# Optimization experiments

Measured on AMD Instinct MI355X. Metric: run time of the kernel, lower is better.

## Reference

```python
import jax, jax.numpy as jnp
import numpy as np

B, T, I, H, O = 128, 512, 128, 256, 1

def setup_inputs() -> dict:
    key = jax.random.key(0)
    ks = jax.random.split(key, 7)
    s_ih = 1.0 / np.sqrt(H)
    return {
        "x": jax.random.normal(ks[0], (B, T, I), dtype=jnp.float32),
        "W_ih": jax.random.uniform(ks[1], (H, I), minval=-s_ih, maxval=s_ih, dtype=jnp.float32),
        "W_hh": jax.random.uniform(ks[2], (H, H), minval=-s_ih, maxval=s_ih, dtype=jnp.float32),
        "b_ih": jax.random.uniform(ks[3], (H,), minval=-s_ih, maxval=s_ih, dtype=jnp.float32),
        "b_hh": jax.random.uniform(ks[4], (H,), minval=-s_ih, maxval=s_ih, dtype=jnp.float32),
        "W_fc": jax.random.uniform(ks[5], (O, H), minval=-s_ih, maxval=s_ih, dtype=jnp.float32),
        "b_fc": jax.random.uniform(ks[6], (O,), minval=-s_ih, maxval=s_ih, dtype=jnp.float32),
    }

def reference(x, W_ih, W_hh, b_ih, b_hh, W_fc, b_fc):
    # Precompute input projections for all timesteps: [B, T, H]
    xp = jnp.einsum("bti,hi->bth", x, W_ih) + b_ih + b_hh
    h0 = jnp.zeros((x.shape[0], W_hh.shape[0]), dtype=x.dtype)

    def step(h, xp_t):
        h_new = jnp.tanh(xp_t + h @ W_hh.T)
        return h_new, None

    # scan over time axis; only final hidden state is needed
    h_last, _ = jax.lax.scan(step, h0, jnp.swapaxes(xp, 0, 1))
    logits = h_last @ W_fc.T + b_fc
    return jax.nn.sigmoid(logits)
```

## Files before the change

kernel.cpp:

```cpp
#include <hip/hip_runtime.h>
#include <hip/hip_bf16.h>


#define B_ 128
#define T_ 512
#define I_ 128
#define H_ 256
#define SCALE 2.8853900817779268f
#define WSC 2032.0f
#define HSC 127.0f
#define SCOMB (SCALE / (WSC * HSC))

typedef __attribute__((ext_vector_type(8))) short short8;
typedef __attribute__((ext_vector_type(4))) float floatx4;
typedef __attribute__((ext_vector_type(4))) int int4v;

__device__ __forceinline__ short8 pack8(float4 lo, float4 hi) {
    __hip_bfloat162 p0 = __float22bfloat162_rn(float2{lo.x, lo.y});
    __hip_bfloat162 p1 = __float22bfloat162_rn(float2{lo.z, lo.w});
    __hip_bfloat162 p2 = __float22bfloat162_rn(float2{hi.x, hi.y});
    __hip_bfloat162 p3 = __float22bfloat162_rn(float2{hi.z, hi.w});
    int4 i;
    i.x = *(int*)&p0; i.y = *(int*)&p1; i.z = *(int*)&p2; i.w = *(int*)&p3;
    return *(short8*)&i;
}
__device__ __forceinline__ short8 pack8s(float4 lo, float4 hi, float s) {
    lo.x *= s; lo.y *= s; lo.z *= s; lo.w *= s;
    hi.x *= s; hi.y *= s; hi.z *= s; hi.w *= s;
    return pack8(lo, hi);
}
__device__ __forceinline__ float tanh_s(float v) {
    float e = __builtin_amdgcn_exp2f(v);
    float r = __builtin_amdgcn_rcpf(e + 1.0f);
    return __builtin_fmaf(-2.0f, r, 1.0f);
}
__device__ __forceinline__ int q4(float a, float b, float c, float d, float s) {
    int qa = (int)rintf(a * s) & 255;
    int qb = (int)rintf(b * s) & 255;
    int qc = (int)rintf(c * s) & 255;
    int qd = (int)rintf(d * s) & 255;
    return qa | (qb << 8) | (qc << 16) | (qd << 24);
}

#define XP_GRID 256
#define XP_NT   ((B_ * T_ / 16) / XP_GRID)
__global__ __launch_bounds__(256, 1)
void xp_kernel(const float* __restrict__ x, const float* __restrict__ W_ih,
               const float* __restrict__ b_ih, const float* __restrict__ b_hh,
               float* __restrict__ xp) {
    const int tid  = threadIdx.x;
    const int wave = tid >> 6, lane = tid & 63;
    const int l15  = lane & 15, quad = lane >> 4;
    const int n0   = wave * 64;

    short8 wfrag[4][4];
#pragma unroll
    for (int mtt = 0; mtt < 4; ++mtt)
#pragma unroll
        for (int kq = 0; kq < 4; ++kq) {
            const float* p = W_ih + (long)(n0 + mtt * 16 + l15) * I_ + kq * 32 + quad * 8;
            wfrag[mtt][kq] = pack8s(*(const float4*)p, *(const float4*)(p + 4), SCALE);
        }
    floatx4 biasv[4];
#pragma unroll
    for (int mtt = 0; mtt < 4; ++mtt)
#pragma unroll
        for (int r = 0; r < 4; ++r) {
            int n = n0 + mtt * 16 + quad * 4 + r;
            biasv[mtt][r] = SCALE * (b_ih[n] + b_hh[n]);
        }

    const long mbase = (long)blockIdx.x * XP_NT * 16;

    float4 qa[4][2], qb[4][2];
#define LDX(Q, IT)                                                              \
    {                                                                           \
        const int itc = ((IT) < XP_NT) ? (IT) : (XP_NT - 1);                    \
        const float* p = x + (mbase + (long)itc * 16 + l15) * I_ + quad * 8;    \
        _Pragma("unroll")                                                       \
        for (int kq = 0; kq < 4; ++kq) {                                        \
            Q[kq][0] = *(const float4*)(p + kq * 32);                           \
            Q[kq][1] = *(const float4*)(p + kq * 32 + 4);                       \
        }                                                                       \
    }
#define ITER(Q, IT, ILD)                                                        \
    {                                                                           \
        short8 xf[4];                                                           \
        _Pragma("unroll")                                                       \
        for (int kq = 0; kq < 4; ++kq) xf[kq] = pack8(Q[kq][0], Q[kq][1]);      \
        LDX(Q, ILD);                                                            \
        floatx4 acc[4];                                                         \
        _Pragma("unroll")                                                       \
        for (int mtt = 0; mtt < 4; ++mtt) acc[mtt] = biasv[mtt];                \
        _Pragma("unroll")                                                       \
        for (int kq = 0; kq < 4; ++kq)                                          \
            _Pragma("unroll")                                                   \
            for (int mtt = 0; mtt < 4; ++mtt)                                   \
                acc[mtt] = __builtin_amdgcn_mfma_f32_16x16x32_bf16(             \
                    wfrag[mtt][kq], xf[kq], acc[mtt], 0, 0, 0);                 \
        float* o = xp + (mbase + (long)(IT) * 16 + l15) * H_ + n0 + quad * 4;   \
        _Pragma("unroll")                                                       \
        for (int mtt = 0; mtt < 4; ++mtt) {                                     \
            float4 st = {acc[mtt][0], acc[mtt][1], acc[mtt][2], acc[mtt][3]};   \
            *(float4*)(o + mtt * 16) = st;                                      \
        }                                                                       \
    }

    LDX(qa, 0);
    LDX(qb, 1);
#pragma unroll 1
    for (int it = 0; it < XP_NT; it += 2) {
        ITER(qa, it, it + 2);
        ITER(qb, it + 1, it + 3);
    }
#undef ITER
#undef LDX
}

__global__ __launch_bounds__(512, 2)
void rnn_kernel(const float* __restrict__ xp, const float* __restrict__ W_hh,
                const float* __restrict__ W_fc, const float* __restrict__ b_fc,
                float* __restrict__ out) {
    __shared__ __align__(16) signed char hbuf[2][16][256];
    const int tid  = threadIdx.x;
    const int wave = tid >> 6, lane = tid & 63;
    const int l15  = lane & 15, quad = lane >> 4;
    const int b0   = blockIdx.x * 16;
    const int n0   = wave * 32;
    const int swz  = l15 & 7;

    int4v wfrag[2][4];
#pragma unroll
    for (int mt = 0; mt < 2; ++mt)
#pragma unroll
        for (int kq = 0; kq < 4; ++kq) {
            const float* p = W_hh + (long)(n0 + mt * 16 + l15) * H_ + kq * 64 + quad * 16;
            int4v f;
#pragma unroll
            for (int j = 0; j < 4; ++j) {
                float4 w = *(const float4*)(p + j * 4);
                f[j] = q4(w.x, w.y, w.z, w.w, WSC);
            }
            wfrag[mt][kq] = f;
        }

    {
        int* hz = (int*)&hbuf[0][0][0];
#pragma unroll
        for (int i = tid; i < 2 * 16 * 256 / 4; i += 512) hz[i] = 0;
    }

    int roff[4];
#pragma unroll
    for (int kq = 0; kq < 4; ++kq)
        roff[kq] = l15 * 256 + (((kq * 4 + quad) ^ swz) << 4);
    int woff[2];
#pragma unroll
    for (int mt = 0; mt < 2; ++mt) {
        int c = wave * 2 + mt;
        woff[mt] = l15 * 256 + ((c ^ swz) << 4) + quad * 4;
    }

    const float* xpl = xp + (long)(b0 + l15) * T_ * H_ + n0 + quad * 4;
    float4 xvA0 = *(const float4*)(xpl);
    float4 xvA1 = *(const float4*)(xpl + 16);
    float4 xvB0 = *(const float4*)(xpl + H_);
    float4 xvB1 = *(const float4*)(xpl + H_ + 16);

    __syncthreads();

    const signed char* hb0r = &hbuf[0][0][0]; signed char* hb0w = &hbuf[0][0][0];
    const signed char* hb1r = &hbuf[1][0][0]; signed char* hb1w = &hbuf[1][0][0];

#define BAR() asm volatile("s_waitcnt lgkmcnt(0)\n\ts_barrier" ::: "memory")

#define STEP(HR, HW, XV0, XV1, TLD)                                             \
    {                                                                           \
                  \
        int4v hfrag[4];                                                         \
        _Pragma("unroll")                                                       \
        for (int kq = 0; kq < 4; ++kq)                                          \
            hfrag[kq] = *(const int4v*)((HR) + roff[kq]);                       \
               \
        float4 xc0 = XV0, xc1 = XV1;                                            \
        XV0 = *(const float4*)(xpl + (long)(TLD) * H_);                         \
        XV1 = *(const float4*)(xpl + (long)(TLD) * H_ + 16);                    \
                                    \
        int4v aC[2], aZ[2];                                                     \
        _Pragma("unroll")                                                       \
        for (int mt = 0; mt < 2; ++mt) {                                        \
            aC[mt] = (int4v){0, 0, 0, 0};                                       \
            aZ[mt] = (int4v){0, 0, 0, 0};                                       \
        }                                                                       \
        _Pragma("unroll")                                                       \
        for (int mt = 0; mt < 2; ++mt) {                                        \
            aC[mt] = __builtin_amdgcn_mfma_i32_16x16x64_i8(                     \
                wfrag[mt][0], hfrag[0], aC[mt], 0, 0, 0);                       \
            aZ[mt] = __builtin_amdgcn_mfma_i32_16x16x64_i8(                     \
                wfrag[mt][2], hfrag[2], aZ[mt], 0, 0, 0);                       \
            aC[mt] = __builtin_amdgcn_mfma_i32_16x16x64_i8(                     \
                wfrag[mt][1], hfrag[1], aC[mt], 0, 0, 0);                       \
            aZ[mt] = __builtin_amdgcn_mfma_i32_16x16x64_i8(                     \
                wfrag[mt][3], hfrag[3], aZ[mt], 0, 0, 0);                       \
        }                                                                       \
             \
        _Pragma("unroll")                                                       \
        for (int mt = 0; mt < 2; ++mt) {                                        \
            float4 xc = (mt == 0) ? xc0 : xc1;                                  \
            float r0 = tanh_s(__builtin_fmaf((float)(aC[mt][0] + aZ[mt][0]), SCOMB, xc.x)); \
            float r1 = tanh_s(__builtin_fmaf((float)(aC[mt][1] + aZ[mt][1]), SCOMB, xc.y)); \
            float r2 = tanh_s(__builtin_fmaf((float)(aC[mt][2] + aZ[mt][2]), SCOMB, xc.z)); \
            float r3 = tanh_s(__builtin_fmaf((float)(aC[mt][3] + aZ[mt][3]), SCOMB, xc.w)); \
            *(int*)((HW) + woff[mt]) = q4(r0, r1, r2, r3, HSC);                 \
        }                                                                       \
        BAR();                                                                  \
    }

#pragma unroll 1
    for (int t = 0; t < T_; t += 2) {
        const int tl0 = (t + 2 < T_) ? t + 2 : T_ - 1;
        const int tl1 = (t + 3 < T_) ? t + 3 : T_ - 1;
        STEP(hb0r, hb1w, xvA0, xvA1, tl0);
        STEP(hb1r, hb0w, xvB0, xvB1, tl1);
    }
#undef STEP
#undef BAR

    if (tid < 256) {
        const int bl = tid >> 4, seg = tid & 15;
        const int bswz = bl & 7;
        const signed char* hr = &hbuf[0][0][0] + bl * 256 + ((seg ^ bswz) << 4);
        float p = 0.0f;
#pragma unroll
        for (int i = 0; i < 16; ++i)
            p += (float)hr[i] * W_fc[seg * 16 + i];
#pragma unroll
        for (int off = 1; off < 16; off <<= 1) p += __shfl_xor(p, off);
        if (seg == 0)
            out[b0 + bl] = 1.0f / (1.0f + __expf(-(p * (1.0f / HSC) + b_fc[0])));
    }
}

extern "C" void kernel_launch(void* const* d_in, const int* in_sizes, int n_in,
                              void* d_out, int out_size, void* d_ws, size_t ws_size,
                              hipStream_t stream) {
    const float* x    = (const float*)d_in[0];
    const float* W_ih = (const float*)d_in[1];
    const float* W_hh = (const float*)d_in[2];
    const float* b_ih = (const float*)d_in[3];
    const float* b_hh = (const float*)d_in[4];
    const float* W_fc = (const float*)d_in[5];
    const float* b_fc = (const float*)d_in[6];
    float* out = (float*)d_out;

    float* xp = (float*)d_ws;

    xp_kernel<<<XP_GRID, 256, 0, stream>>>(x, W_ih, b_ih, b_hh, xp);
    rnn_kernel<<<B_ / 16, 512, 0, stream>>>(xp, W_hh, W_fc, b_fc, out);
}
```

Before: 396.0 us.

## Pre-quantize input projection to int32 MFMA accumulator scale and fuse tanh-quantize

The input projection is now stored as int32 values pre-scaled by the weight times hidden quantization scale, so the recurrent step can seed the int8 MFMA accumulator directly with it. This removes the separate aZ accumulator chain, the per-element float add, and the fmaf in the serial loop. The tanh plus int8 quantization is fused into one fma using a magic-number float trick, with byte extraction done via v_perm instead of rintf, mask and shift. This shortens the latency-bound per-timestep critical path. The cost is a longer serial chain of four dependent MFMAs per accumulator and extra rounding error in the input projection.

```diff
diff --git a/kernel.cpp b/kernel.cpp
--- a/kernel.cpp
+++ b/kernel.cpp
@@ -9,7 +9,9 @@
 #define SCALE 2.8853900817779268f
 #define WSC 2032.0f
 #define HSC 127.0f
-#define SCOMB (SCALE / (WSC * HSC))
+#define WHS (WSC * HSC)
+#define SCOMB (SCALE / WHS)
+#define MAGICQ 12583039.0f
 
 typedef __attribute__((ext_vector_type(8))) short short8;
 typedef __attribute__((ext_vector_type(4))) float floatx4;
@@ -24,16 +26,6 @@
     i.x = *(int*)&p0; i.y = *(int*)&p1; i.z = *(int*)&p2; i.w = *(int*)&p3;
     return *(short8*)&i;
 }
-__device__ __forceinline__ short8 pack8s(float4 lo, float4 hi, float s) {
-    lo.x *= s; lo.y *= s; lo.z *= s; lo.w *= s;
-    hi.x *= s; hi.y *= s; hi.z *= s; hi.w *= s;
-    return pack8(lo, hi);
-}
-__device__ __forceinline__ float tanh_s(float v) {
-    float e = __builtin_amdgcn_exp2f(v);
-    float r = __builtin_amdgcn_rcpf(e + 1.0f);
-    return __builtin_fmaf(-2.0f, r, 1.0f);
-}
 __device__ __forceinline__ int q4(float a, float b, float c, float d, float s) {
     int qa = (int)rintf(a * s) & 255;
     int qb = (int)rintf(b * s) & 255;
@@ -47,7 +39,7 @@
 __global__ __launch_bounds__(256, 1)
 void xp_kernel(const float* __restrict__ x, const float* __restrict__ W_ih,
                const float* __restrict__ b_ih, const float* __restrict__ b_hh,
-               float* __restrict__ xp) {
+               int* __restrict__ xq) {
     const int tid  = threadIdx.x;
     const int wave = tid >> 6, lane = tid & 63;
     const int l15  = lane & 15, quad = lane >> 4;
@@ -59,7 +51,7 @@
 #pragma unroll
         for (int kq = 0; kq < 4; ++kq) {
             const float* p = W_ih + (long)(n0 + mtt * 16 + l15) * I_ + kq * 32 + quad * 8;
-            wfrag[mtt][kq] = pack8s(*(const float4*)p, *(const float4*)(p + 4), SCALE);
+            wfrag[mtt][kq] = pack8(*(const float4*)p, *(const float4*)(p + 4));
         }
     floatx4 biasv[4];
 #pragma unroll
@@ -67,7 +59,7 @@
 #pragma unroll
         for (int r = 0; r < 4; ++r) {
             int n = n0 + mtt * 16 + quad * 4 + r;
-            biasv[mtt][r] = SCALE * (b_ih[n] + b_hh[n]);
+            biasv[mtt][r] = b_ih[n] + b_hh[n];
         }
 
     const long mbase = (long)blockIdx.x * XP_NT * 16;
@@ -98,11 +90,15 @@
             for (int mtt = 0; mtt < 4; ++mtt)                                   \
                 acc[mtt] = __builtin_amdgcn_mfma_f32_16x16x32_bf16(             \
                     wfrag[mtt][kq], xf[kq], acc[mtt], 0, 0, 0);                 \
-        float* o = xp + (mbase + (long)(IT) * 16 + l15) * H_ + n0 + quad * 4;   \
+        int* o = xq + (mbase + (long)(IT) * 16 + l15) * H_ + n0 + quad * 4;     \
         _Pragma("unroll")                                                       \
         for (int mtt = 0; mtt < 4; ++mtt) {                                     \
-            float4 st = {acc[mtt][0], acc[mtt][1], acc[mtt][2], acc[mtt][3]};   \
-            *(float4*)(o + mtt * 16) = st;                                      \
+            int4 st;                                                            \
+            st.x = (int)rintf(acc[mtt][0] * WHS);                               \
+            st.y = (int)rintf(acc[mtt][1] * WHS);                               \
+            st.z = (int)rintf(acc[mtt][2] * WHS);                               \
+            st.w = (int)rintf(acc[mtt][3] * WHS);                               \
+            *(int4*)(o + mtt * 16) = st;                                        \
         }                                                                       \
     }
 
@@ -118,7 +114,7 @@
 }
 
 __global__ __launch_bounds__(512, 2)
-void rnn_kernel(const float* __restrict__ xp, const float* __restrict__ W_hh,
+void rnn_kernel(const int* __restrict__ xq, const float* __restrict__ W_hh,
                 const float* __restrict__ W_fc, const float* __restrict__ b_fc,
                 float* __restrict__ out) {
     __shared__ __align__(16) signed char hbuf[2][16][256];
@@ -161,11 +157,11 @@
         woff[mt] = l15 * 256 + ((c ^ swz) << 4) + quad * 4;
     }
 
-    const float* xpl = xp + (long)(b0 + l15) * T_ * H_ + n0 + quad * 4;
-    float4 xvA0 = *(const float4*)(xpl);
-    float4 xvA1 = *(const float4*)(xpl + 16);
-    float4 xvB0 = *(const float4*)(xpl + H_);
-    float4 xvB1 = *(const float4*)(xpl + H_ + 16);
+    const int* xql = xq + (long)(b0 + l15) * T_ * H_ + n0 + quad * 4;
+    int4v xvA0 = *(const int4v*)(xql);
+    int4v xvA1 = *(const int4v*)(xql + 16);
+    int4v xvB0 = *(const int4v*)(xql + H_);
+    int4v xvB1 = *(const int4v*)(xql + H_ + 16);
 
     __syncthreads();
 
@@ -174,44 +170,44 @@
 
 #define BAR() asm volatile("s_waitcnt lgkmcnt(0)\n\ts_barrier" ::: "memory")
 
+#define TQ(ACCI)                                                                \
+    ({                                                                          \
+        float v_ = (float)(ACCI) * SCOMB;                                       \
+        float e_ = __builtin_amdgcn_exp2f(v_);                                  \
+        float rc_ = __builtin_amdgcn_rcpf(e_ + 1.0f);                           \
+        __builtin_fmaf(-254.0f, rc_, MAGICQ);                                   \
+    })
+
 #define STEP(HR, HW, XV0, XV1, TLD)                                             \
     {                                                                           \
-                  \
+                      \
         int4v hfrag[4];                                                         \
         _Pragma("unroll")                                                       \
         for (int kq = 0; kq < 4; ++kq)                                          \
             hfrag[kq] = *(const int4v*)((HR) + roff[kq]);                       \
-               \
-        float4 xc0 = XV0, xc1 = XV1;                                            \
-        XV0 = *(const float4*)(xpl + (long)(TLD) * H_);                         \
-        XV1 = *(const float4*)(xpl + (long)(TLD) * H_ + 16);                    \
-                                    \
-        int4v aC[2], aZ[2];                                                     \
+                           \
+        int4v aC[2];                                                            \
+        aC[0] = XV0; aC[1] = XV1;                                               \
+        XV0 = *(const int4v*)(xql + (long)(TLD) * H_);                          \
+        XV1 = *(const int4v*)(xql + (long)(TLD) * H_ + 16);                     \
+                   \
+        _Pragma("unroll")                                                       \
+        for (int kq = 0; kq < 4; ++kq)                                          \
+            _Pragma("unroll")                                                   \
+            for (int mt = 0; mt < 2; ++mt)                                      \
+                aC[mt] = __builtin_amdgcn_mfma_i32_16x16x64_i8(                 \
+                    wfrag[mt][kq], hfrag[kq], aC[mt], 0, 0, 0);                 \
+             \
         _Pragma("unroll")                                                       \
         for (int mt = 0; mt < 2; ++mt) {                                        \
-            aC[mt] = (int4v){0, 0, 0, 0};                                       \
-            aZ[mt] = (int4v){0, 0, 0, 0};                                       \
-        }                                                                       \
-        _Pragma("unroll")                                                       \
-        for (int mt = 0; mt < 2; ++mt) {                                        \
-            aC[mt] = __builtin_amdgcn_mfma_i32_16x16x64_i8(                     \
-                wfrag[mt][0], hfrag[0], aC[mt], 0, 0, 0);                       \
-            aZ[mt] = __builtin_amdgcn_mfma_i32_16x16x64_i8(                     \
-                wfrag[mt][2], hfrag[2], aZ[mt], 0, 0, 0);                       \
-            aC[mt] = __builtin_amdgcn_mfma_i32_16x16x64_i8(                     \
-                wfrag[mt][1], hfrag[1], aC[mt], 0, 0, 0);                       \
-            aZ[mt] = __builtin_amdgcn_mfma_i32_16x16x64_i8(                     \
-                wfrag[mt][3], hfrag[3], aZ[mt], 0, 0, 0);                       \
-        }                                                                       \
-             \
-        _Pragma("unroll")                                                       \
-        for (int mt = 0; mt < 2; ++mt) {                                        \
-            float4 xc = (mt == 0) ? xc0 : xc1;                                  \
-            float r0 = tanh_s(__builtin_fmaf((float)(aC[mt][0] + aZ[mt][0]), SCOMB, xc.x)); \
-            float r1 = tanh_s(__builtin_fmaf((float)(aC[mt][1] + aZ[mt][1]), SCOMB, xc.y)); \
-            float r2 = tanh_s(__builtin_fmaf((float)(aC[mt][2] + aZ[mt][2]), SCOMB, xc.z)); \
-            float r3 = tanh_s(__builtin_fmaf((float)(aC[mt][3] + aZ[mt][3]), SCOMB, xc.w)); \
-            *(int*)((HW) + woff[mt]) = q4(r0, r1, r2, r3, HSC);                 \
+            float f0 = TQ(aC[mt][0]);                                           \
+            float f1 = TQ(aC[mt][1]);                                           \
+            float f2 = TQ(aC[mt][2]);                                           \
+            float f3 = TQ(aC[mt][3]);                                           \
+            unsigned t01 = __builtin_amdgcn_perm(*(unsigned*)&f1, *(unsigned*)&f0, 0x00000400u); \
+            unsigned t23 = __builtin_amdgcn_perm(*(unsigned*)&f3, *(unsigned*)&f2, 0x00000400u); \
+            unsigned pk  = __builtin_amdgcn_perm(t23, t01, 0x05040100u);        \
+            *(int*)((HW) + woff[mt]) = (int)pk;                                 \
         }                                                                       \
         BAR();                                                                  \
     }
@@ -224,6 +220,7 @@
         STEP(hb1r, hb0w, xvB0, xvB1, tl1);
     }
 #undef STEP
+#undef TQ
 #undef BAR
 
     if (tid < 256) {
@@ -253,8 +250,8 @@
     const float* b_fc = (const float*)d_in[6];
     float* out = (float*)d_out;
 
-    float* xp = (float*)d_ws;
-
-    xp_kernel<<<XP_GRID, 256, 0, stream>>>(x, W_ih, b_ih, b_hh, xp);
-    rnn_kernel<<<B_ / 16, 512, 0, stream>>>(xp, W_hh, W_fc, b_fc, out);
-}
+    int* xq = (int*)d_ws;
+
+    xp_kernel<<<XP_GRID, 256, 0, stream>>>(x, W_ih, b_ih, b_hh, xq);
+    rnn_kernel<<<B_ / 16, 512, 0, stream>>>(xq, W_hh, W_fc, b_fc, out);
+}
```

Result: faster. 357.7 us (-9.7%).
